# Performance work log

Hardware: AMD Instinct MI355X
Metric: run time of the kernel (lower is better)

Reference implementation:

```python
import jax, jax.numpy as jnp
import numpy as np

N = 100_000   # nodes
E = 1_600_000 # edges
F = 128       # num_features
D = 32        # hidden dim
G = 1000      # graphs (segments for global_add_pool)
C = 10        # num_classes
BN_EPS = 1e-5


def setup_inputs() -> dict:
    key = jax.random.key(0)
    ks = jax.random.split(key, 16)
    sc = 0.05
    x = jax.random.normal(ks[0], (N, F), jnp.float32)
    edge_index = jax.random.randint(ks[1], (2, E), 0, N)
    batch = jnp.sort(jax.random.randint(ks[2], (N,), 0, G))
    # layer-1 MLP: F -> D -> D
    W1a = jax.random.normal(ks[3], (F, D), jnp.float32) * sc
    b1a = jnp.zeros((D,), jnp.float32)
    W1b = jax.random.normal(ks[4], (D, D), jnp.float32) * sc
    b1b = jnp.zeros((D,), jnp.float32)
    # layers 2-5 MLPs stacked: D -> D -> D
    Wa = jax.random.normal(ks[5], (4, D, D), jnp.float32) * sc
    ba = jnp.zeros((4, D), jnp.float32)
    Wb = jax.random.normal(ks[6], (4, D, D), jnp.float32) * sc
    bb = jnp.zeros((4, D), jnp.float32)
    # BatchNorm affine params for 5 BN layers
    gamma = jnp.ones((5, D), jnp.float32)
    beta = jnp.zeros((5, D), jnp.float32)
    fc1_w = jax.random.normal(ks[7], (D, D), jnp.float32) * sc
    fc1_b = jnp.zeros((D,), jnp.float32)
    fc2_w = jax.random.normal(ks[8], (D, C), jnp.float32) * sc
    fc2_b = jnp.zeros((C,), jnp.float32)
    return dict(x=x, edge_index=edge_index, batch=batch,
                W1a=W1a, b1a=b1a, W1b=W1b, b1b=b1b,
                Wa=Wa, ba=ba, Wb=Wb, bb=bb,
                gamma=gamma, beta=beta,
                fc1_w=fc1_w, fc1_b=fc1_b, fc2_w=fc2_w, fc2_b=fc2_b)


def _gin_conv(h, src, dst, wa, ba_, wb, bb_):
    # GINConv (eps=0): nn(x + sum_{j->i} x_j); messages flow src=row0 -> dst=row1
    agg = jax.ops.segment_sum(h[src], dst, num_segments=N)
    h = h + agg
    h = jnp.maximum(h @ wa + ba_, 0.0) @ wb + bb_
    return h


def _bn(h, g, b):
    # BatchNorm1d, training-mode batch stats (biased variance)
    m = h.mean(axis=0)
    v = h.var(axis=0)
    return g * (h - m) * jax.lax.rsqrt(v + BN_EPS) + b


def reference(x, edge_index, batch, W1a, b1a, W1b, b1b, Wa, ba, Wb, bb,
              gamma, beta, fc1_w, fc1_b, fc2_w, fc2_b):
    src, dst = edge_index[0], edge_index[1]
    h = jnp.maximum(_gin_conv(x, src, dst, W1a, b1a, W1b, b1b), 0.0)
    h = _bn(h, gamma[0], beta[0])
    for i in range(4):  # fixed small layer count
        h = jnp.maximum(_gin_conv(h, src, dst, Wa[i], ba[i], Wb[i], bb[i]), 0.0)
        h = _bn(h, gamma[i + 1], beta[i + 1])
    # global_add_pool over graphs
    pooled = jax.ops.segment_sum(h, batch, num_segments=G)  # [G, D]
    h = jnp.maximum(pooled @ fc1_w + fc1_b, 0.0)
    # dropout is identity in eval mode
    logits = h @ fc2_w + fc2_b
    return jax.nn.log_softmax(logits, axis=-1)
```

## Files before the change

### kernel.cpp

```cpp
#include <hip/hip_runtime.h>
#include <hip/hip_bf16.h>
#include <hip/hip_fp16.h>

#define NN 100000
#define EE 1600000
#define FF 128
#define DD 32
#define GG 1000
#define CC 10
#define BN_EPS 1e-5f
#define REC 48
#define CAPE 47
#define NB64 1563

#define NBUCK 98
#define BSH 10
#define BCAP 17280
#define CCAP 64
#define CHUNK 2048
#define NCHUNK 782
#define NZBLK 127

typedef int   vint4   __attribute__((ext_vector_type(4)));
typedef float vfloat4 __attribute__((ext_vector_type(4)));

__device__ __forceinline__ void up8(uint4 u, float* f) {
    __half2* h = (__half2*)&u;
#pragma unroll
    for (int i = 0; i < 4; i++) {
        float2 t = __half22float2(h[i]);
        f[2 * i] = t.x; f[2 * i + 1] = t.y;
    }
}

__device__ __forceinline__ void acc8(float* acc, uint4 u) {
    __half2* h = (__half2*)&u;
#pragma unroll
    for (int i = 0; i < 4; i++) {
        float2 t = __half22float2(h[i]);
        acc[2 * i] += t.x; acc[2 * i + 1] += t.y;
    }
}

__device__ __forceinline__ int gather_node(float* acc, const uint4* __restrict__ V4,
                                           const int* __restrict__ sp, int sub) {
    vint4 h = *(const vint4*)sp;
    int deg = h.x; if (deg > CAPE) deg = CAPE;
    if (deg >= 3) {
        uint4 u0 = V4[(long)h.y * 4 + sub];
        uint4 u1 = V4[(long)h.z * 4 + sub];
        uint4 u2 = V4[(long)h.w * 4 + sub];
        acc8(acc, u0); acc8(acc, u1); acc8(acc, u2);
        const int* q = sp + 4;
        int rem = deg - 3;
        int i = 0;
        for (; i + 8 <= rem; i += 8) {
            vint4 sa = *(const vint4*)(q + i);
            vint4 sb = *(const vint4*)(q + i + 4);
            uint4 v0 = V4[(long)sa.x * 4 + sub];
            uint4 v1 = V4[(long)sa.y * 4 + sub];
            uint4 v2 = V4[(long)sa.z * 4 + sub];
            uint4 v3 = V4[(long)sa.w * 4 + sub];
            uint4 v4 = V4[(long)sb.x * 4 + sub];
            uint4 v5 = V4[(long)sb.y * 4 + sub];
            uint4 v6 = V4[(long)sb.z * 4 + sub];
            uint4 v7 = V4[(long)sb.w * 4 + sub];
            acc8(acc, v0); acc8(acc, v1); acc8(acc, v2); acc8(acc, v3);
            acc8(acc, v4); acc8(acc, v5); acc8(acc, v6); acc8(acc, v7);
        }
        for (; i + 4 <= rem; i += 4) {
            vint4 ss = *(const vint4*)(q + i);
            uint4 v0 = V4[(long)ss.x * 4 + sub];
            uint4 v1 = V4[(long)ss.y * 4 + sub];
            uint4 v2 = V4[(long)ss.z * 4 + sub];
            uint4 v3 = V4[(long)ss.w * 4 + sub];
            acc8(acc, v0); acc8(acc, v1); acc8(acc, v2); acc8(acc, v3);
        }
        for (; i < rem; i++) acc8(acc, V4[(long)q[i] * 4 + sub]);
    } else {
        if (deg >= 1) acc8(acc, V4[(long)h.y * 4 + sub]);
        if (deg >= 2) acc8(acc, V4[(long)h.z * 4 + sub]);
    }
    return deg;
}

__global__ __launch_bounds__(256) void k_bin(const int* __restrict__ src,
                                             const int* __restrict__ dst,
                                             int* __restrict__ gcur,
                                             int* __restrict__ pack,
                                             float* __restrict__ zeroS) {
    int tid = threadIdx.x;
    int bid = blockIdx.x;
    if (bid >= NCHUNK) {
        int idx = (bid - NCHUNK) * 256 + tid;
        if (idx < 32320) zeroS[idx] = 0.f;
        return;
    }
    __shared__ int bcnt[NBUCK];
    __shared__ int bbase[NBUCK];
    __shared__ int bbuf[NBUCK * CCAP];
    for (int i = tid; i < NBUCK; i += 256) bcnt[i] = 0;
    __syncthreads();
    int e0 = bid * CHUNK;
#pragma unroll
    for (int i = 0; i < CHUNK / 256; i++) {
        int e = e0 + i * 256 + tid;
        if (e < EE) {
            int d = __builtin_nontemporal_load(dst + e);
            int s = __builtin_nontemporal_load(src + e);
            int b = d >> BSH;
            int p = atomicAdd(&bcnt[b], 1);
            if (p < CCAP) bbuf[b * CCAP + p] = ((d & ((1 << BSH) - 1)) << 17) | s;
        }
    }
    __syncthreads();
    for (int b = tid; b < NBUCK; b += 256) {
        int c = bcnt[b]; if (c > CCAP) c = CCAP;
        bbase[b] = atomicAdd(&gcur[b], c);
    }
    __syncthreads();
    int grp = tid >> 5, lane = tid & 31;
    for (int b = grp; b < NBUCK; b += 8) {
        int c = bcnt[b]; if (c > CCAP) c = CCAP;
        int gb = bbase[b];
        for (int i = lane; i < c; i += 32) {
            int idx = gb + i;
            if (idx >= 0 && idx < BCAP)
                __builtin_nontemporal_store(bbuf[b * CCAP + i], pack + b * BCAP + idx);
        }
    }
}

__global__ __launch_bounds__(256) void k_prep2(const int* __restrict__ gcur,
                                               const int* __restrict__ pack,
                                               int* __restrict__ rec,
                                               const float* __restrict__ x,
                                               const float* __restrict__ W,
                                               __half* __restrict__ t) {
    __shared__ float sh[FF * DD + 32 * FF];
    int bid = blockIdx.x, tid = threadIdx.x;
    if (bid < NBUCK) {
        int* lcnt = (int*)sh;
        for (int i = tid; i < (1 << BSH); i += 256) lcnt[i] = 0;
        __syncthreads();
        int m = gcur[bid]; if (m > BCAP) m = BCAP;
        const int* pk = pack + bid * BCAP;
        int nb = bid << BSH;
        for (int i = tid; i < m; i += 256) {
            int w = __builtin_nontemporal_load(pk + i);
            int s = w & 0x1FFFF;
            int dl = w >> 17;
            int p = atomicAdd(&lcnt[dl], 1);
            if (p < CAPE) rec[(nb + dl) * REC + 1 + p] = s;
        }
        __syncthreads();
        for (int dl = tid; dl < (1 << BSH); dl += 256) {
            int d = nb + dl;
            if (d < NN) rec[d * REC] = lcnt[dl];
        }
    } else {
        float* Wl = sh;
        float* xs = sh + FF * DD;
        int gid = bid - NBUCK;
        const float4* W4 = (const float4*)W;
        float4* Wl4 = (float4*)Wl;
        for (int i = tid; i < FF * DD / 4; i += 256) Wl4[i] = W4[i];
        long node0 = (long)gid * 32;
        const vfloat4* x4 = (const vfloat4*)(x + node0 * FF);
        vfloat4* xs4 = (vfloat4*)xs;
        for (int i = tid; i < 32 * FF / 4; i += 256)
            xs4[i] = __builtin_nontemporal_load(x4 + i);
        __syncthreads();
        int tx = tid & 31, ty = tid >> 5;
        float a0 = 0.f, a1 = 0.f, a2 = 0.f, a3 = 0.f;
#pragma unroll 8
        for (int k = 0; k < FF; k++) {
            float w = Wl[k * DD + tx];
            a0 += xs[ty * FF + k] * w;
            a1 += xs[(ty + 8) * FF + k] * w;
            a2 += xs[(ty + 16) * FF + k] * w;
            a3 += xs[(ty + 24) * FF + k] * w;
        }
        t[(node0 + ty) * DD + tx] = __float2half_rn(a0);
        t[(node0 + ty + 8) * DD + tx] = __float2half_rn(a1);
        t[(node0 + ty + 16) * DD + tx] = __float2half_rn(a2);
        t[(node0 + ty + 24) * DD + tx] = __float2half_rn(a3);
    }
}

__global__ __launch_bounds__(256) void k_fused1(const uint4* __restrict__ T4,
                                                const int* __restrict__ rec,
                                                const float* __restrict__ b1a,
                                                const float* __restrict__ W1b,
                                                const float* __restrict__ b1b,
                                                __half* __restrict__ vout,
                                                float* __restrict__ S) {
    __shared__ float U[64 * DD];
    __shared__ float ssum[DD], ssq[DD];
    int tid = threadIdx.x;
    if (tid < DD) { ssum[tid] = 0.f; ssq[tid] = 0.f; }
    int g4 = tid >> 2, sub = tid & 3;
    int n = blockIdx.x * 64 + g4;
    if (n < NN) {
        float acc[8];
        up8(T4[(long)n * 4 + sub], acc);
        gather_node(acc, T4, rec + n * REC, sub);
#pragma unroll
        for (int j = 0; j < 8; j++)
            U[g4 * DD + sub * 8 + j] = fmaxf(acc[j] + b1a[sub * 8 + j], 0.f);
    } else {
#pragma unroll
        for (int j = 0; j < 8; j++) U[g4 * DD + sub * 8 + j] = 0.f;
    }
    __syncthreads();
    int tx = tid & 31, ty = tid >> 5;
    float w[DD];
#pragma unroll
    for (int k = 0; k < DD; k++) w[k] = W1b[k * DD + tx];
    float bb = b1b[tx];
    float sl = 0.f, sq = 0.f;
#pragma unroll
    for (int m = 0; m < 8; m++) {
        int node = ty + 8 * m;
        int nn = blockIdx.x * 64 + node;
        float a = bb;
        const float4* h4 = (const float4*)(U + node * DD);
#pragma unroll
        for (int k4 = 0; k4 < 8; k4++) {
            float4 h = h4[k4];
            a += h.x * w[4 * k4] + h.y * w[4 * k4 + 1] + h.z * w[4 * k4 + 2] + h.w * w[4 * k4 + 3];
        }
        if (nn < NN) {
            float hv = fmaxf(a, 0.f);
            vout[(long)nn * DD + tx] = __float2half_rn(hv);
            sl += hv; sq += hv * hv;
        }
    }
    atomicAdd(&ssum[tx], sl);
    atomicAdd(&ssq[tx], sq);
    __syncthreads();
    if (tid < DD) {
        unsafeAtomicAdd(&S[tid], ssum[tid]);
        unsafeAtomicAdd(&S[DD + tid], ssq[tid]);
    }
}

__global__ __launch_bounds__(256) void k_fusedN(const uint4* __restrict__ Vin4,
                                                const int* __restrict__ rec,
                                                const float* __restrict__ Sprev,
                                                const float* __restrict__ gamma,
                                                const float* __restrict__ beta,
                                                const float* __restrict__ wa,
                                                const float* __restrict__ ba,
                                                const float* __restrict__ wb,
                                                const float* __restrict__ bb,
                                                __half* __restrict__ vout,
                                                float* __restrict__ S) {
    __shared__ float Hs[64 * DD];
    __shared__ float U[64 * DD];
    __shared__ float ssum[DD], ssq[DD], scl[DD], shl[DD];
    int tid = threadIdx.x;
    if (tid < DD) {
        ssum[tid] = 0.f; ssq[tid] = 0.f;
        float mean = Sprev[tid] * (1.0f / NN);
        float var = Sprev[DD + tid] * (1.0f / NN) - mean * mean;
        float inv = rsqrtf(var + BN_EPS);
        float sc = gamma[tid] * inv;
        scl[tid] = sc;
        shl[tid] = beta[tid] - mean * sc;
    }
    __syncthreads();
    int g4 = tid >> 2, sub = tid & 3;
    int n = blockIdx.x * 64 + g4;
    if (n < NN) {
        float acc[8];
        up8(Vin4[(long)n * 4 + sub], acc);
        int deg = gather_node(acc, Vin4, rec + n * REC, sub);
        float d1 = (float)(1 + deg);
#pragma unroll
        for (int j = 0; j < 8; j++) {
            int f = sub * 8 + j;
            Hs[g4 * DD + f] = scl[f] * acc[j] + d1 * shl[f];
        }
    } else {
#pragma unroll
        for (int j = 0; j < 8; j++) Hs[g4 * DD + sub * 8 + j] = 0.f;
    }
    __syncthreads();
    int tx = tid & 31, ty = tid >> 5;
    {
        float w[DD];
#pragma unroll
        for (int k = 0; k < DD; k++) w[k] = wa[k * DD + tx];
        float bal = ba[tx];
#pragma unroll
        for (int m = 0; m < 8; m++) {
            int node = ty + 8 * m;
            float a = bal;
            const float4* h4 = (const float4*)(Hs + node * DD);
#pragma unroll
            for (int k4 = 0; k4 < 8; k4++) {
                float4 h = h4[k4];
                a += h.x * w[4 * k4] + h.y * w[4 * k4 + 1] + h.z * w[4 * k4 + 2] + h.w * w[4 * k4 + 3];
            }
            U[node * DD + tx] = fmaxf(a, 0.f);
        }
    }
    __syncthreads();
    {
        float w[DD];
#pragma unroll
        for (int k = 0; k < DD; k++) w[k] = wb[k * DD + tx];
        float bbl = bb[tx];
        float sl = 0.f, sq = 0.f;
#pragma unroll
        for (int m = 0; m < 8; m++) {
            int node = ty + 8 * m;
            int nn = blockIdx.x * 64 + node;
            float a = bbl;
            const float4* h4 = (const float4*)(U + node * DD);
#pragma unroll
            for (int k4 = 0; k4 < 8; k4++) {
                float4 h = h4[k4];
                a += h.x * w[4 * k4] + h.y * w[4 * k4 + 1] + h.z * w[4 * k4 + 2] + h.w * w[4 * k4 + 3];
            }
            if (nn < NN) {
                float hv = fmaxf(a, 0.f);
                vout[(long)nn * DD + tx] = __float2half_rn(hv);
                sl += hv; sq += hv * hv;
            }
        }
        atomicAdd(&ssum[tx], sl);
        atomicAdd(&ssq[tx], sq);
    }
    __syncthreads();
    if (tid < DD) {
        unsafeAtomicAdd(&S[tid], ssum[tid]);
        unsafeAtomicAdd(&S[DD + tid], ssq[tid]);
    }
}

__global__ __launch_bounds__(256) void k_pool(const __half* __restrict__ v,
                                              const float* __restrict__ Sprev,
                                              const float* __restrict__ gamma,
                                              const float* __restrict__ beta,
                                              const int* __restrict__ batch,
                                              float* __restrict__ pooled) {
    __shared__ float scl[DD], shl[DD];
    int tid = threadIdx.x;
    if (tid < DD) {
        float mean = Sprev[tid] * (1.0f / NN);
        float var = Sprev[DD + tid] * (1.0f / NN) - mean * mean;
        float inv = rsqrtf(var + BN_EPS);
        float sc = gamma[tid] * inv;
        scl[tid] = sc;
        shl[tid] = beta[tid] - mean * sc;
    }
    __syncthreads();
    int tx = tid & 31, ty = tid >> 5;
    float sc = scl[tx], sh = shl[tx];
    int n0 = blockIdx.x * 256 + ty * 32;
    const unsigned short* vu = (const unsigned short*)v;
    int cur = -1; float run = 0.f;
    for (int i = 0; i < 32; i++) {
        int n = n0 + i;
        if (n >= NN) break;
        int b = __builtin_nontemporal_load(batch + n);
        float val = __half2float(__ushort_as_half(
                        __builtin_nontemporal_load(vu + (long)n * DD + tx))) * sc + sh;
        if (b != cur) {
            if (cur >= 0) unsafeAtomicAdd(&pooled[(long)cur * DD + tx], run);
            run = 0.f; cur = b;
        }
        run += val;
    }
    if (cur >= 0) unsafeAtomicAdd(&pooled[(long)cur * DD + tx], run);
}

__global__ __launch_bounds__(256) void k_head(const float* __restrict__ pooled,
                                              const float* __restrict__ fc1w,
                                              const float* __restrict__ fc1b,
                                              const float* __restrict__ fc2w,
                                              const float* __restrict__ fc2b,
                                              float* __restrict__ out) {
    __shared__ float W1[DD * DD], B1[DD], W2[DD * CC], B2[CC];
    int tid = threadIdx.x;
    for (int i = tid; i < DD * DD; i += 256) W1[i] = fc1w[i];
    for (int i = tid; i < DD * CC; i += 256) W2[i] = fc2w[i];
    if (tid < DD) B1[tid] = fc1b[tid];
    if (tid < CC) B2[tid] = fc2b[tid];
    __syncthreads();
    int g = blockIdx.x * 256 + tid;
    if (g >= GG) return;
    float p[DD];
#pragma unroll
    for (int d = 0; d < DD; d++) p[d] = pooled[(long)g * DD + d];
    float h[DD];
#pragma unroll
    for (int d = 0; d < DD; d++) {
        float acc = B1[d];
#pragma unroll
        for (int k = 0; k < DD; k++) acc += p[k] * W1[k * DD + d];
        h[d] = fmaxf(acc, 0.f);
    }
    float lg[CC];
#pragma unroll
    for (int c = 0; c < CC; c++) {
        float acc = B2[c];
#pragma unroll
        for (int d = 0; d < DD; d++) acc += h[d] * W2[d * CC + c];
        lg[c] = acc;
    }
    float m = lg[0];
#pragma unroll
    for (int c = 1; c < CC; c++) m = fmaxf(m, lg[c]);
    float s = 0.f;
#pragma unroll
    for (int c = 0; c < CC; c++) s += __expf(lg[c] - m);
    float ls = logf(s);
#pragma unroll
    for (int c = 0; c < CC; c++) out[(long)g * CC + c] = lg[c] - m - ls;
}

extern "C" void kernel_launch(void* const* d_in, const int* in_sizes, int n_in,
                              void* d_out, int out_size, void* d_ws, size_t ws_size,
                              hipStream_t stream) {
    const float* x    = (const float*)d_in[0];
    const int* ei     = (const int*)d_in[1];
    const int* batch  = (const int*)d_in[2];
    const float* W1a  = (const float*)d_in[3];
    const float* b1a  = (const float*)d_in[4];
    const float* W1b  = (const float*)d_in[5];
    const float* b1b  = (const float*)d_in[6];
    const float* Wa   = (const float*)d_in[7];
    const float* ba   = (const float*)d_in[8];
    const float* Wb   = (const float*)d_in[9];
    const float* bb   = (const float*)d_in[10];
    const float* gm   = (const float*)d_in[11];
    const float* bt   = (const float*)d_in[12];
    const float* fc1w = (const float*)d_in[13];
    const float* fc1b = (const float*)d_in[14];
    const float* fc2w = (const float*)d_in[15];
    const float* fc2b = (const float*)d_in[16];

    char* base = (char*)d_ws;
    __half* Th   = (__half*)base;
    __half* Vh   = (__half*)(base + 6400000);
    int*    pack = (int*)(base + 6400000);
    float*  S    = (float*)(base + 13173760);
    float*  POOL = (float*)(base + 13175040);
    int*    gcur = (int*)(base + 13303040);
    int*    rec  = (int*)(base + 13303552);

    const int* esrc = ei;
    const int* edst = ei + EE;

    hipMemsetAsync(gcur, 0, 512, stream);

    k_bin<<<NCHUNK + NZBLK, 256, 0, stream>>>(esrc, edst, gcur, pack, S);

    k_prep2<<<NBUCK + 3125, 256, 0, stream>>>(gcur, pack, rec, x, W1a, Th);

    k_fused1<<<NB64, 256, 0, stream>>>((const uint4*)Th, rec,
                                       b1a, W1b, b1b, Vh, S);

    __half* bufs[2] = {Vh, Th};
    for (int j = 0; j < 4; j++) {
        k_fusedN<<<NB64, 256, 0, stream>>>((const uint4*)bufs[j & 1], rec,
                                           S + j * 64, gm + j * 32, bt + j * 32,
                                           Wa + j * 1024, ba + j * 32,
                                           Wb + j * 1024, bb + j * 32,
                                           bufs[(j + 1) & 1], S + (j + 1) * 64);
    }

    k_pool<<<(NN + 255) / 256, 256, 0, stream>>>(Vh, S + 4 * 64, gm + 4 * 32,
                                                 bt + 4 * 32, batch, POOL);
    k_head<<<(GG + 255) / 256, 256, 0, stream>>>(POOL, fc1w, fc1b, fc2w, fc2b,
                                                 (float*)d_out);
}
```

Measured before the change: 529.4 us.

## Gather two nodes per thread group and halve block size in fused GIN kernels

Each 4-thread group now gathers neighbor rows for two nodes at once, interleaving their loads to raise memory-level parallelism. Blocks shrink from 256 to 128 threads, and the dense MLP stage processes 16 nodes per thread row instead of 8. This trades extra registers and lower thread count for more independent outstanding loads per thread. Divergence rises when the two nodes' degrees differ.

```diff
diff --git a/kernel.cpp b/kernel.cpp
--- a/kernel.cpp
+++ b/kernel.cpp
@@ -42,46 +42,97 @@
     }
 }
 
-__device__ __forceinline__ int gather_node(float* acc, const uint4* __restrict__ V4,
-                                           const int* __restrict__ sp, int sub) {
-    vint4 h = *(const vint4*)sp;
-    int deg = h.x; if (deg > CAPE) deg = CAPE;
+__device__ __forceinline__ void drain8(float* acc, const uint4* __restrict__ V4,
+                                       const int* __restrict__ q, int i, int rem, int sub) {
+    for (; i + 8 <= rem; i += 8) {
+        vint4 sa = *(const vint4*)(q + i);
+        vint4 sb = *(const vint4*)(q + i + 4);
+        uint4 v0 = V4[(long)sa.x * 4 + sub];
+        uint4 v1 = V4[(long)sa.y * 4 + sub];
+        uint4 v2 = V4[(long)sa.z * 4 + sub];
+        uint4 v3 = V4[(long)sa.w * 4 + sub];
+        uint4 v4 = V4[(long)sb.x * 4 + sub];
+        uint4 v5 = V4[(long)sb.y * 4 + sub];
+        uint4 v6 = V4[(long)sb.z * 4 + sub];
+        uint4 v7 = V4[(long)sb.w * 4 + sub];
+        acc8(acc, v0); acc8(acc, v1); acc8(acc, v2); acc8(acc, v3);
+        acc8(acc, v4); acc8(acc, v5); acc8(acc, v6); acc8(acc, v7);
+    }
+    for (; i + 4 <= rem; i += 4) {
+        vint4 ss = *(const vint4*)(q + i);
+        uint4 v0 = V4[(long)ss.x * 4 + sub];
+        uint4 v1 = V4[(long)ss.y * 4 + sub];
+        uint4 v2 = V4[(long)ss.z * 4 + sub];
+        uint4 v3 = V4[(long)ss.w * 4 + sub];
+        acc8(acc, v0); acc8(acc, v1); acc8(acc, v2); acc8(acc, v3);
+    }
+    for (; i < rem; i++) acc8(acc, V4[(long)q[i] * 4 + sub]);
+}
+
+__device__ __forceinline__ void gather_one(float* acc, const uint4* __restrict__ V4,
+                                           vint4 h, const int* __restrict__ sp,
+                                           int deg, int sub) {
     if (deg >= 3) {
         uint4 u0 = V4[(long)h.y * 4 + sub];
         uint4 u1 = V4[(long)h.z * 4 + sub];
         uint4 u2 = V4[(long)h.w * 4 + sub];
         acc8(acc, u0); acc8(acc, u1); acc8(acc, u2);
-        const int* q = sp + 4;
-        int rem = deg - 3;
-        int i = 0;
-        for (; i + 8 <= rem; i += 8) {
-            vint4 sa = *(const vint4*)(q + i);
-            vint4 sb = *(const vint4*)(q + i + 4);
-            uint4 v0 = V4[(long)sa.x * 4 + sub];
-            uint4 v1 = V4[(long)sa.y * 4 + sub];
-            uint4 v2 = V4[(long)sa.z * 4 + sub];
-            uint4 v3 = V4[(long)sa.w * 4 + sub];
-            uint4 v4 = V4[(long)sb.x * 4 + sub];
-            uint4 v5 = V4[(long)sb.y * 4 + sub];
-            uint4 v6 = V4[(long)sb.z * 4 + sub];
-            uint4 v7 = V4[(long)sb.w * 4 + sub];
-            acc8(acc, v0); acc8(acc, v1); acc8(acc, v2); acc8(acc, v3);
-            acc8(acc, v4); acc8(acc, v5); acc8(acc, v6); acc8(acc, v7);
-        }
-        for (; i + 4 <= rem; i += 4) {
-            vint4 ss = *(const vint4*)(q + i);
-            uint4 v0 = V4[(long)ss.x * 4 + sub];
-            uint4 v1 = V4[(long)ss.y * 4 + sub];
-            uint4 v2 = V4[(long)ss.z * 4 + sub];
-            uint4 v3 = V4[(long)ss.w * 4 + sub];
-            acc8(acc, v0); acc8(acc, v1); acc8(acc, v2); acc8(acc, v3);
-        }
-        for (; i < rem; i++) acc8(acc, V4[(long)q[i] * 4 + sub]);
+        drain8(acc, V4, sp + 4, 0, deg - 3, sub);
     } else {
         if (deg >= 1) acc8(acc, V4[(long)h.y * 4 + sub]);
         if (deg >= 2) acc8(acc, V4[(long)h.z * 4 + sub]);
     }
-    return deg;
+}
+
+__device__ __forceinline__ void gather_pair(float* accA, float* accB,
+                                            const uint4* __restrict__ V4,
+                                            const int* __restrict__ spA,
+                                            const int* __restrict__ spB,
+                                            int sub, bool hasB,
+                                            int& degAo, int& degBo) {
+    vint4 hA = *(const vint4*)spA;
+    int degA = hA.x > CAPE ? CAPE : hA.x;
+    vint4 hB{};
+    int degB = 0;
+    if (hasB) { hB = *(const vint4*)spB; degB = hB.x > CAPE ? CAPE : hB.x; }
+    degAo = degA; degBo = degB;
+    if (degA >= 3 && degB >= 3) {
+        uint4 a0 = V4[(long)hA.y * 4 + sub];
+        uint4 b0 = V4[(long)hB.y * 4 + sub];
+        uint4 a1 = V4[(long)hA.z * 4 + sub];
+        uint4 b1 = V4[(long)hB.z * 4 + sub];
+        uint4 a2 = V4[(long)hA.w * 4 + sub];
+        uint4 b2 = V4[(long)hB.w * 4 + sub];
+        acc8(accA, a0); acc8(accB, b0);
+        acc8(accA, a1); acc8(accB, b1);
+        acc8(accA, a2); acc8(accB, b2);
+        const int* qA = spA + 4;
+        const int* qB = spB + 4;
+        int remA = degA - 3, remB = degB - 3;
+        int ia = 0, ib = 0;
+        while (ia + 4 <= remA && ib + 4 <= remB) {
+            vint4 sa = *(const vint4*)(qA + ia);
+            vint4 sb = *(const vint4*)(qB + ib);
+            uint4 va0 = V4[(long)sa.x * 4 + sub];
+            uint4 vb0 = V4[(long)sb.x * 4 + sub];
+            uint4 va1 = V4[(long)sa.y * 4 + sub];
+            uint4 vb1 = V4[(long)sb.y * 4 + sub];
+            uint4 va2 = V4[(long)sa.z * 4 + sub];
+            uint4 vb2 = V4[(long)sb.z * 4 + sub];
+            uint4 va3 = V4[(long)sa.w * 4 + sub];
+            uint4 vb3 = V4[(long)sb.w * 4 + sub];
+            acc8(accA, va0); acc8(accB, vb0);
+            acc8(accA, va1); acc8(accB, vb1);
+            acc8(accA, va2); acc8(accB, vb2);
+            acc8(accA, va3); acc8(accB, vb3);
+            ia += 4; ib += 4;
+        }
+        drain8(accA, V4, qA, ia, remA, sub);
+        drain8(accB, V4, qB, ib, remB, sub);
+    } else {
+        gather_one(accA, V4, hA, spA, degA, sub);
+        if (hasB) gather_one(accB, V4, hB, spB, degB, sub);
+    }
 }
 
 __global__ __launch_bounds__(256) void k_bin(const int* __restrict__ src,
@@ -188,7 +239,7 @@
     }
 }
 
-__global__ __launch_bounds__(256) void k_fused1(const uint4* __restrict__ T4,
+__global__ __launch_bounds__(128) void k_fused1(const uint4* __restrict__ T4,
                                                 const int* __restrict__ rec,
                                                 const float* __restrict__ b1a,
                                                 const float* __restrict__ W1b,
@@ -199,18 +250,30 @@
     __shared__ float ssum[DD], ssq[DD];
     int tid = threadIdx.x;
     if (tid < DD) { ssum[tid] = 0.f; ssq[tid] = 0.f; }
-    int g4 = tid >> 2, sub = tid & 3;
-    int n = blockIdx.x * 64 + g4;
-    if (n < NN) {
-        float acc[8];
-        up8(T4[(long)n * 4 + sub], acc);
-        gather_node(acc, T4, rec + n * REC, sub);
+    int p = tid >> 2, sub = tid & 3;
+    int base = blockIdx.x * 64;
+    int nA = base + p;
+    int nB = base + 32 + p;
+    bool hasB = nB < NN;
+    {
+        float accA[8], accB[8];
+        up8(T4[(long)nA * 4 + sub], accA);
+        if (hasB) up8(T4[(long)nB * 4 + sub], accB);
+        else { for (int j = 0; j < 8; j++) accB[j] = 0.f; }
+        int degA, degB;
+        gather_pair(accA, accB, T4, rec + nA * REC, rec + (long)nB * REC,
+                    sub, hasB, degA, degB);
 #pragma unroll
         for (int j = 0; j < 8; j++)
-            U[g4 * DD + sub * 8 + j] = fmaxf(acc[j] + b1a[sub * 8 + j], 0.f);
-    } else {
-#pragma unroll
-        for (int j = 0; j < 8; j++) U[g4 * DD + sub * 8 + j] = 0.f;
+            U[p * DD + sub * 8 + j] = fmaxf(accA[j] + b1a[sub * 8 + j], 0.f);
+        if (hasB) {
+#pragma unroll
+            for (int j = 0; j < 8; j++)
+                U[(32 + p) * DD + sub * 8 + j] = fmaxf(accB[j] + b1a[sub * 8 + j], 0.f);
+        } else {
+#pragma unroll
+            for (int j = 0; j < 8; j++) U[(32 + p) * DD + sub * 8 + j] = 0.f;
+        }
     }
     __syncthreads();
     int tx = tid & 31, ty = tid >> 5;
@@ -220,9 +283,9 @@
     float bb = b1b[tx];
     float sl = 0.f, sq = 0.f;
 #pragma unroll
-    for (int m = 0; m < 8; m++) {
-        int node = ty + 8 * m;
-        int nn = blockIdx.x * 64 + node;
+    for (int m = 0; m < 16; m++) {
+        int node = m * 4 + ty;
+        int nn = base + node;
         float a = bb;
         const float4* h4 = (const float4*)(U + node * DD);
 #pragma unroll
@@ -245,7 +308,7 @@
     }
 }
 
-__global__ __launch_bounds__(256) void k_fusedN(const uint4* __restrict__ Vin4,
+__global__ __launch_bounds__(128) void k_fusedN(const uint4* __restrict__ Vin4,
                                                 const int* __restrict__ rec,
                                                 const float* __restrict__ Sprev,
                                                 const float* __restrict__ gamma,
@@ -270,21 +333,36 @@
         shl[tid] = beta[tid] - mean * sc;
     }
     __syncthreads();
-    int g4 = tid >> 2, sub = tid & 3;
-    int n = blockIdx.x * 64 + g4;
-    if (n < NN) {
-        float acc[8];
-        up8(Vin4[(long)n * 4 + sub], acc);
-        int deg = gather_node(acc, Vin4, rec + n * REC, sub);
-        float d1 = (float)(1 + deg);
+    int p = tid >> 2, sub = tid & 3;
+    int base = blockIdx.x * 64;
+    int nA = base + p;
+    int nB = base + 32 + p;
+    bool hasB = nB < NN;
+    {
+        float accA[8], accB[8];
+        up8(Vin4[(long)nA * 4 + sub], accA);
+        if (hasB) up8(Vin4[(long)nB * 4 + sub], accB);
+        else { for (int j = 0; j < 8; j++) accB[j] = 0.f; }
+        int degA, degB;
+        gather_pair(accA, accB, Vin4, rec + nA * REC, rec + (long)nB * REC,
+                    sub, hasB, degA, degB);
+        float d1A = (float)(1 + degA);
+        float d1B = (float)(1 + degB);
 #pragma unroll
         for (int j = 0; j < 8; j++) {
             int f = sub * 8 + j;
-            Hs[g4 * DD + f] = scl[f] * acc[j] + d1 * shl[f];
-        }
-    } else {
-#pragma unroll
-        for (int j = 0; j < 8; j++) Hs[g4 * DD + sub * 8 + j] = 0.f;
+            Hs[p * DD + f] = scl[f] * accA[j] + d1A * shl[f];
+        }
+        if (hasB) {
+#pragma unroll
+            for (int j = 0; j < 8; j++) {
+                int f = sub * 8 + j;
+                Hs[(32 + p) * DD + f] = scl[f] * accB[j] + d1B * shl[f];
+            }
+        } else {
+#pragma unroll
+            for (int j = 0; j < 8; j++) Hs[(32 + p) * DD + sub * 8 + j] = 0.f;
+        }
     }
     __syncthreads();
     int tx = tid & 31, ty = tid >> 5;
@@ -294,8 +372,8 @@
         for (int k = 0; k < DD; k++) w[k] = wa[k * DD + tx];
         float bal = ba[tx];
 #pragma unroll
-        for (int m = 0; m < 8; m++) {
-            int node = ty + 8 * m;
+        for (int m = 0; m < 16; m++) {
+            int node = m * 4 + ty;
             float a = bal;
             const float4* h4 = (const float4*)(Hs + node * DD);
 #pragma unroll
@@ -314,9 +392,9 @@
         float bbl = bb[tx];
         float sl = 0.f, sq = 0.f;
 #pragma unroll
-        for (int m = 0; m < 8; m++) {
-            int node = ty + 8 * m;
-            int nn = blockIdx.x * 64 + node;
+        for (int m = 0; m < 16; m++) {
+            int node = m * 4 + ty;
+            int nn = base + node;
             float a = bbl;
             const float4* h4 = (const float4*)(U + node * DD);
 #pragma unroll
@@ -461,12 +539,12 @@
 
     k_prep2<<<NBUCK + 3125, 256, 0, stream>>>(gcur, pack, rec, x, W1a, Th);
 
-    k_fused1<<<NB64, 256, 0, stream>>>((const uint4*)Th, rec,
+    k_fused1<<<NB64, 128, 0, stream>>>((const uint4*)Th, rec,
                                        b1a, W1b, b1b, Vh, S);
 
     __half* bufs[2] = {Vh, Th};
     for (int j = 0; j < 4; j++) {
-        k_fusedN<<<NB64, 256, 0, stream>>>((const uint4*)bufs[j & 1], rec,
+        k_fusedN<<<NB64, 128, 0, stream>>>((const uint4*)bufs[j & 1], rec,
                                            S + j * 64, gm + j * 32, bt + j * 32,
                                            Wa + j * 1024, ba + j * 32,
                                            Wb + j * 1024, bb + j * 32,
```

Measured after the change: 558.5 us. 5.5% more time.

## Partition neighbor lists by source half, pad global counters, overlap gather with BN setup

Applied to the files above, without the earlier changes.

Each node's adjacency record is now split into neighbors with source below and above N/2, with a packed header holding total and low counts. The gather visits the two halves in sequence, which is meant to improve cache locality of the feature reads. Per-bucket global counters are padded to separate cache lines to reduce atomic contention. The layer-N kernel now starts the gather before the BN scale and shift setup and its barrier. Costs are a second counting pass over the packed edges in prep and the loss of vectorized index loads in the gather.

```diff
diff --git a/kernel.cpp b/kernel.cpp
--- a/kernel.cpp
+++ b/kernel.cpp
@@ -12,6 +12,7 @@
 #define REC 48
 #define CAPE 47
 #define NB64 1563
+#define NHALF 50000
 
 #define NBUCK 98
 #define BSH 10
@@ -20,6 +21,7 @@
 #define CHUNK 2048
 #define NCHUNK 782
 #define NZBLK 127
+#define GCSTRIDE 16
 
 typedef int   vint4   __attribute__((ext_vector_type(4)));
 typedef float vfloat4 __attribute__((ext_vector_type(4)));
@@ -42,46 +44,43 @@
     }
 }
 
+__device__ __forceinline__ void gather_list(float* acc, const uint4* __restrict__ V4,
+                                            const int* __restrict__ q, int cnt, int sub) {
+    int i = 0;
+    for (; i + 8 <= cnt; i += 8) {
+        int s0 = q[i], s1 = q[i + 1], s2 = q[i + 2], s3 = q[i + 3];
+        int s4 = q[i + 4], s5 = q[i + 5], s6 = q[i + 6], s7 = q[i + 7];
+        uint4 v0 = V4[(long)s0 * 4 + sub];
+        uint4 v1 = V4[(long)s1 * 4 + sub];
+        uint4 v2 = V4[(long)s2 * 4 + sub];
+        uint4 v3 = V4[(long)s3 * 4 + sub];
+        uint4 v4 = V4[(long)s4 * 4 + sub];
+        uint4 v5 = V4[(long)s5 * 4 + sub];
+        uint4 v6 = V4[(long)s6 * 4 + sub];
+        uint4 v7 = V4[(long)s7 * 4 + sub];
+        acc8(acc, v0); acc8(acc, v1); acc8(acc, v2); acc8(acc, v3);
+        acc8(acc, v4); acc8(acc, v5); acc8(acc, v6); acc8(acc, v7);
+    }
+    if (i + 4 <= cnt) {
+        int s0 = q[i], s1 = q[i + 1], s2 = q[i + 2], s3 = q[i + 3];
+        uint4 v0 = V4[(long)s0 * 4 + sub];
+        uint4 v1 = V4[(long)s1 * 4 + sub];
+        uint4 v2 = V4[(long)s2 * 4 + sub];
+        uint4 v3 = V4[(long)s3 * 4 + sub];
+        acc8(acc, v0); acc8(acc, v1); acc8(acc, v2); acc8(acc, v3);
+        i += 4;
+    }
+    for (; i < cnt; i++) acc8(acc, V4[(long)q[i] * 4 + sub]);
+}
+
 __device__ __forceinline__ int gather_node(float* acc, const uint4* __restrict__ V4,
                                            const int* __restrict__ sp, int sub) {
-    vint4 h = *(const vint4*)sp;
-    int deg = h.x; if (deg > CAPE) deg = CAPE;
-    if (deg >= 3) {
-        uint4 u0 = V4[(long)h.y * 4 + sub];
-        uint4 u1 = V4[(long)h.z * 4 + sub];
-        uint4 u2 = V4[(long)h.w * 4 + sub];
-        acc8(acc, u0); acc8(acc, u1); acc8(acc, u2);
-        const int* q = sp + 4;
-        int rem = deg - 3;
-        int i = 0;
-        for (; i + 8 <= rem; i += 8) {
-            vint4 sa = *(const vint4*)(q + i);
-            vint4 sb = *(const vint4*)(q + i + 4);
-            uint4 v0 = V4[(long)sa.x * 4 + sub];
-            uint4 v1 = V4[(long)sa.y * 4 + sub];
-            uint4 v2 = V4[(long)sa.z * 4 + sub];
-            uint4 v3 = V4[(long)sa.w * 4 + sub];
-            uint4 v4 = V4[(long)sb.x * 4 + sub];
-            uint4 v5 = V4[(long)sb.y * 4 + sub];
-            uint4 v6 = V4[(long)sb.z * 4 + sub];
-            uint4 v7 = V4[(long)sb.w * 4 + sub];
-            acc8(acc, v0); acc8(acc, v1); acc8(acc, v2); acc8(acc, v3);
-            acc8(acc, v4); acc8(acc, v5); acc8(acc, v6); acc8(acc, v7);
-        }
-        for (; i + 4 <= rem; i += 4) {
-            vint4 ss = *(const vint4*)(q + i);
-            uint4 v0 = V4[(long)ss.x * 4 + sub];
-            uint4 v1 = V4[(long)ss.y * 4 + sub];
-            uint4 v2 = V4[(long)ss.z * 4 + sub];
-            uint4 v3 = V4[(long)ss.w * 4 + sub];
-            acc8(acc, v0); acc8(acc, v1); acc8(acc, v2); acc8(acc, v3);
-        }
-        for (; i < rem; i++) acc8(acc, V4[(long)q[i] * 4 + sub]);
-    } else {
-        if (deg >= 1) acc8(acc, V4[(long)h.y * 4 + sub]);
-        if (deg >= 2) acc8(acc, V4[(long)h.z * 4 + sub]);
-    }
-    return deg;
+    int hdr = sp[0];
+    int tot = hdr & 0xFF; if (tot > CAPE) tot = CAPE;
+    int lo = (hdr >> 8) & 0xFF; if (lo > tot) lo = tot;
+    gather_list(acc, V4, sp + 1, lo, sub);
+    gather_list(acc, V4, sp + 1 + lo, tot - lo, sub);
+    return tot;
 }
 
 __global__ __launch_bounds__(256) void k_bin(const int* __restrict__ src,
@@ -116,7 +115,7 @@
     __syncthreads();
     for (int b = tid; b < NBUCK; b += 256) {
         int c = bcnt[b]; if (c > CCAP) c = CCAP;
-        bbase[b] = atomicAdd(&gcur[b], c);
+        bbase[b] = atomicAdd(&gcur[b * GCSTRIDE], c);
     }
     __syncthreads();
     int grp = tid >> 5, lane = tid & 31;
@@ -140,23 +139,45 @@
     __shared__ float sh[FF * DD + 32 * FF];
     int bid = blockIdx.x, tid = threadIdx.x;
     if (bid < NBUCK) {
-        int* lcnt = (int*)sh;
-        for (int i = tid; i < (1 << BSH); i += 256) lcnt[i] = 0;
+        int* lcnt_lo = (int*)sh;
+        int* lcnt_to = lcnt_lo + 1024;
+        int* lcur_lo = lcnt_to + 1024;
+        int* lcur_hi = lcur_lo + 1024;
+        for (int i = tid; i < (1 << BSH); i += 256) { lcnt_lo[i] = 0; lcnt_to[i] = 0; }
         __syncthreads();
-        int m = gcur[bid]; if (m > BCAP) m = BCAP;
+        int m = gcur[bid * GCSTRIDE]; if (m > BCAP) m = BCAP;
         const int* pk = pack + bid * BCAP;
         int nb = bid << BSH;
         for (int i = tid; i < m; i += 256) {
-            int w = __builtin_nontemporal_load(pk + i);
+            int w = pk[i];
             int s = w & 0x1FFFF;
             int dl = w >> 17;
-            int p = atomicAdd(&lcnt[dl], 1);
+            atomicAdd(&lcnt_to[dl], 1);
+            if (s < NHALF) atomicAdd(&lcnt_lo[dl], 1);
+        }
+        __syncthreads();
+        for (int dl = tid; dl < (1 << BSH); dl += 256) {
+            int lo = lcnt_lo[dl]; if (lo > CAPE) lo = CAPE;
+            lcur_lo[dl] = 0;
+            lcur_hi[dl] = lo;
+        }
+        __syncthreads();
+        for (int i = tid; i < m; i += 256) {
+            int w = pk[i];
+            int s = w & 0x1FFFF;
+            int dl = w >> 17;
+            int p = (s < NHALF) ? atomicAdd(&lcur_lo[dl], 1)
+                                : atomicAdd(&lcur_hi[dl], 1);
             if (p < CAPE) rec[(nb + dl) * REC + 1 + p] = s;
         }
         __syncthreads();
         for (int dl = tid; dl < (1 << BSH); dl += 256) {
             int d = nb + dl;
-            if (d < NN) rec[d * REC] = lcnt[dl];
+            if (d < NN) {
+                int tot = lcnt_to[dl]; if (tot > CAPE) tot = CAPE;
+                int lo = lcnt_lo[dl]; if (lo > tot) lo = tot;
+                rec[d * REC] = tot | (lo << 8);
+            }
         }
     } else {
         float* Wl = sh;
@@ -202,9 +223,10 @@
     int g4 = tid >> 2, sub = tid & 3;
     int n = blockIdx.x * 64 + g4;
     if (n < NN) {
+        const int* sp = rec + (long)n * REC;
         float acc[8];
         up8(T4[(long)n * 4 + sub], acc);
-        gather_node(acc, T4, rec + n * REC, sub);
+        gather_node(acc, T4, sp, sub);
 #pragma unroll
         for (int j = 0; j < 8; j++)
             U[g4 * DD + sub * 8 + j] = fmaxf(acc[j] + b1a[sub * 8 + j], 0.f);
@@ -260,6 +282,16 @@
     __shared__ float U[64 * DD];
     __shared__ float ssum[DD], ssq[DD], scl[DD], shl[DD];
     int tid = threadIdx.x;
+    int g4 = tid >> 2, sub = tid & 3;
+    int n = blockIdx.x * 64 + g4;
+    float acc[8];
+    int deg = 0;
+    bool valid = n < NN;
+    if (valid) {
+        const int* sp = rec + (long)n * REC;
+        up8(Vin4[(long)n * 4 + sub], acc);
+        deg = gather_node(acc, Vin4, sp, sub);
+    }
     if (tid < DD) {
         ssum[tid] = 0.f; ssq[tid] = 0.f;
         float mean = Sprev[tid] * (1.0f / NN);
@@ -270,12 +302,7 @@
         shl[tid] = beta[tid] - mean * sc;
     }
     __syncthreads();
-    int g4 = tid >> 2, sub = tid & 3;
-    int n = blockIdx.x * 64 + g4;
-    if (n < NN) {
-        float acc[8];
-        up8(Vin4[(long)n * 4 + sub], acc);
-        int deg = gather_node(acc, Vin4, rec + n * REC, sub);
+    if (valid) {
         float d1 = (float)(1 + deg);
 #pragma unroll
         for (int j = 0; j < 8; j++) {
@@ -450,12 +477,12 @@
     float*  S    = (float*)(base + 13173760);
     float*  POOL = (float*)(base + 13175040);
     int*    gcur = (int*)(base + 13303040);
-    int*    rec  = (int*)(base + 13303552);
+    int*    rec  = (int*)(base + 13309440);
 
     const int* esrc = ei;
     const int* edst = ei + EE;
 
-    hipMemsetAsync(gcur, 0, 512, stream);
+    hipMemsetAsync(gcur, 0, 6400, stream);
 
     k_bin<<<NCHUNK + NZBLK, 256, 0, stream>>>(esrc, edst, gcur, pack, S);
 
```

Result: slower. 540.9 us (+2.2%).
